# Kernel tuning notes

Hardware: AMD Instinct MI355X
Metric: run time of the kernel (lower is better)

## Reference

```python
import jax, jax.numpy as jnp
import numpy as np

N_NODES = 100000


def setup_inputs() -> dict:
    key = jax.random.key(0)
    k1, k2, k3, k4, k5 = jax.random.split(key, 5)
    in_f, out_f, E = 128, 128, 1600000
    std = 1.0 / np.sqrt(out_f)
    H = jax.random.normal(k1, (N_NODES, in_f), dtype=jnp.float32)
    W = jax.random.uniform(k2, (in_f, out_f), minval=-std, maxval=std, dtype=jnp.float32)
    bias = jax.random.uniform(k3, (out_f,), minval=-std, maxval=std, dtype=jnp.float32)
    row = jax.random.randint(k4, (E,), 0, N_NODES, dtype=jnp.int32)
    col = jax.random.randint(k5, (E,), 0, N_NODES, dtype=jnp.int32)
    return {"H": H, "W": W, "bias": bias, "row": row, "col": col}


def reference(H, W, bias, row, col):
    # H: [N, in_f]; W: [in_f, out_f]; row/col: [E] edge endpoints
    Hp = jnp.matmul(H, W)  # [N, out_f]
    # edge-wise attention: leaky_relu(<Hp[i], Hp[j]>)
    scores = jax.nn.leaky_relu(jnp.sum(Hp[row] * Hp[col], axis=-1), negative_slope=0.2)  # [E]
    # scatter-softmax over rows (matches sparse_softmax: exp / (row_sum + 1e-10))
    ex = jnp.exp(scores)
    denom = jax.ops.segment_sum(ex, row, num_segments=N_NODES)  # [N]
    attn = ex / (denom[row] + 1e-10)  # [E]
    # sparse-matmul aggregation: out[i] = sum_e attn[e] * Hp[col[e]]
    out = jax.ops.segment_sum(attn[:, None] * Hp[col], row, num_segments=N_NODES)  # [N, out_f]
    return out + bias
```

## Files before the change

kernel.cpp:

```cpp
#include <hip/hip_runtime.h>
#include <hip/hip_bf16.h>

#define RSH 7
#define RPB (1 << RSH)
#define CSH 17
#define CMASK ((1 << CSH) - 1)
#define CHUNK_E 8192
#define CAP 4096
#define NBMAX 1024

typedef __attribute__((ext_vector_type(8))) _Float16 f16x8;
typedef __attribute__((ext_vector_type(2))) _Float16 f16x2;
typedef __attribute__((ext_vector_type(4))) float f32x4;

__device__ __forceinline__ unsigned int pack2h(float a, float b) {
    union { _Float16 h[2]; unsigned int u; } c;
    c.h[0] = (_Float16)a; c.h[1] = (_Float16)b;
    return c.u;
}
__device__ __forceinline__ unsigned short f2h_bits(float f) {
    union { _Float16 h; unsigned short u; } c;
    c.h = (_Float16)f;
    return c.u;
}

__global__ __launch_bounds__(256) void wsplit(
    const float* __restrict__ Wg, unsigned int* __restrict__ WhiG)
{
    int task = blockIdx.x * 256 + threadIdx.x;
    if (task >= 2048) return;
    int n  = task & 127;
    int k0 = (task >> 7) * 8;
    unsigned int hi[4];
    #pragma unroll
    for (int j = 0; j < 4; ++j) {
        float w0 = Wg[(size_t)(k0 + 2*j)     * 128 + n];
        float w1 = Wg[(size_t)(k0 + 2*j + 1) * 128 + n];
        hi[j] = pack2h(w0, w1);
    }
    int byte = (k0 * 2) ^ ((n & 7) << 4);
    *(uint4*)((char*)WhiG + n * 256 + byte) = make_uint4(hi[0], hi[1], hi[2], hi[3]);
}

__global__ __launch_bounds__(512) void gemm_hist(
    const float* __restrict__ H, const unsigned int* __restrict__ WhiG,
    unsigned short* __restrict__ Hpb, int N,
    const int* __restrict__ row, unsigned short* __restrict__ Ht,
    int E, int nchunk, int nb2, int gemmBlocks)
{
    __shared__ unsigned short Ahi[128 * 128];
    __shared__ unsigned short Whi[128 * 128];
    const int tid = threadIdx.x;

    if (blockIdx.x >= gemmBlocks) {
        int* cnt = (int*)Ahi;
        const int c = blockIdx.x - gemmBlocks;
        for (int i = tid; i < nb2; i += 512) cnt[i] = 0;
        __syncthreads();
        const int e0 = c * CHUNK_E;
        const int e1 = min(e0 + CHUNK_E, E);
        for (int e = e0 + tid; e < e1; e += 512)
            atomicAdd(&cnt[row[e] >> RSH], 1);
        __syncthreads();
        for (int i = tid; i < nb2; i += 512)
            Ht[(size_t)i * nchunk + c] = (unsigned short)cnt[i];
        return;
    }

    const int rbase = blockIdx.x * 128;

    #pragma unroll
    for (int i = 0; i < 4; ++i) {
        int idx = tid + 512 * i;
        ((uint4*)Whi)[idx] = ((const uint4*)WhiG)[idx];
    }
    #pragma unroll
    for (int i = 0; i < 8; ++i) {
        int flat = tid + 512 * i;
        int rr = flat >> 5;
        int c4  = (flat & 31) * 4;
        float4 h = make_float4(0.f, 0.f, 0.f, 0.f);
        if (rbase + rr < N)
            h = *(const float4*)&H[(size_t)(rbase + rr) * 128 + c4];
        uint2 vh;
        vh.x = pack2h(h.x, h.y);
        vh.y = pack2h(h.z, h.w);
        int byte = (c4 * 2) ^ ((rr & 7) << 4);
        *(uint2*)((char*)Ahi + rr * 256 + byte) = vh;
    }
    __syncthreads();

    const int wid = tid >> 6, lane = tid & 63;
    const int wm = wid >> 1, wn = wid & 1;
    const int lr = lane & 15, lg = lane >> 4;
    f32x4 acc[2][4] = {};

    #pragma unroll
    for (int ks = 0; ks < 4; ++ks) {
        const int kb = ks * 64 + lg * 16;
        f16x8 ahi[2];
        #pragma unroll
        for (int mi = 0; mi < 2; ++mi) {
            int rr = wm * 32 + mi * 16 + lr;
            int sw = kb ^ ((rr & 7) << 4);
            ahi[mi] = *(const f16x8*)((char*)Ahi + rr * 256 + sw);
        }
        #pragma unroll
        for (int nf = 0; nf < 4; ++nf) {
            int n = wn * 64 + nf * 16 + lr;
            int sw = kb ^ ((n & 7) << 4);
            f16x8 bhi = *(const f16x8*)((char*)Whi + n * 256 + sw);
            #pragma unroll
            for (int mi = 0; mi < 2; ++mi)
                acc[mi][nf] = __builtin_amdgcn_mfma_f32_16x16x32_f16(ahi[mi], bhi, acc[mi][nf], 0, 0, 0);
        }
    }

    #pragma unroll
    for (int mi = 0; mi < 2; ++mi) {
        #pragma unroll
        for (int nf = 0; nf < 4; ++nf) {
            int col = wn * 64 + nf * 16 + lr;
            #pragma unroll
            for (int i = 0; i < 4; ++i) {
                int rr = rbase + wm * 32 + mi * 16 + lg * 4 + i;
                if (rr < N)
                    Hpb[(size_t)rr * 128 + col] = f2h_bits(acc[mi][nf][i]);
            }
        }
    }
}

__global__ __launch_bounds__(256) void bucket_scan(
    const unsigned short* __restrict__ Ht, unsigned short* __restrict__ rel,
    int* __restrict__ totals, int nchunk)
{
    __shared__ int s[256];
    const int b = blockIdx.x, tid = threadIdx.x;
    int v = (tid < nchunk) ? (int)Ht[(size_t)b * nchunk + tid] : 0;
    s[tid] = v;
    __syncthreads();
    for (int d = 1; d < 256; d <<= 1) {
        int t = (tid >= d) ? s[tid - d] : 0;
        __syncthreads();
        s[tid] += t;
        __syncthreads();
    }
    if (tid < nchunk) rel[(size_t)b * nchunk + tid] = (unsigned short)(s[tid] - v);
    if (tid == 255) totals[b] = s[255];
}

__global__ __launch_bounds__(1024) void bucket_ptr_scan(
    const int* __restrict__ totals, int* __restrict__ bucketptr, int nb2)
{
    __shared__ int s[1024];
    const int tid = threadIdx.x;
    int v = (tid < nb2) ? totals[tid] : 0;
    s[tid] = v;
    __syncthreads();
    for (int d = 1; d < 1024; d <<= 1) {
        int t = (tid >= d) ? s[tid - d] : 0;
        __syncthreads();
        s[tid] += t;
        __syncthreads();
    }
    if (tid < nb2) bucketptr[tid] = s[tid] - v;
    if (tid == nb2 - 1) bucketptr[nb2] = s[tid];
}

__global__ __launch_bounds__(256) void chunk_scatter(
    const int* __restrict__ row, const int* __restrict__ col,
    const unsigned short* __restrict__ rel, const int* __restrict__ bucketptr,
    int* __restrict__ colsort, int E, int nchunk, int nb2)
{
    __shared__ int cur[NBMAX];
    __shared__ int gb[NBMAX];
    const int tid = threadIdx.x;
    const int c = blockIdx.x;
    const int e0 = c * CHUNK_E;
    const int tot = min(CHUNK_E, E - e0);

    for (int b = tid; b < nb2; b += 256) {
        cur[b] = 0;
        gb[b] = bucketptr[b] + (int)rel[(size_t)b * nchunk + c];
    }
    __syncthreads();

    for (int j = tid; j < tot; j += 256) {
        int r = row[e0 + j], cc = col[e0 + j];
        int b = r >> RSH;
        int p = atomicAdd(&cur[b], 1);
        colsort[gb[b] + p] = ((r & (RPB - 1)) << CSH) | cc;
    }
}

__global__ __launch_bounds__(256) void bucket_sort(
    const int* __restrict__ bucketptr, int* __restrict__ rowptr,
    int* __restrict__ colsort, int N)
{
    __shared__ int rcnt[RPB];
    __shared__ int rcur[RPB];
    __shared__ int sc[256];
    __shared__ int ord[CAP];
    const int b = blockIdx.x, tid = threadIdx.x;
    const int rbase = b << RSH;
    const int s0 = bucketptr[b];
    const int cnt = bucketptr[b + 1] - s0;

    if (tid < RPB) rcnt[tid] = 0;
    __syncthreads();
    for (int j = tid; j < cnt; j += 256)
        atomicAdd(&rcnt[colsort[s0 + j] >> CSH], 1);
    __syncthreads();

    int v = (tid < RPB) ? rcnt[tid] : 0;
    sc[tid] = v;
    __syncthreads();
    for (int d = 1; d < RPB; d <<= 1) {
        int t = (tid >= d) ? sc[tid - d] : 0;
        __syncthreads();
        sc[tid] += t;
        __syncthreads();
    }
    if (tid < RPB) {
        int ex = sc[tid] - v;
        rcur[tid] = ex;
        int r = rbase + tid;
        if (r < N) rowptr[r] = s0 + ex;
    }
    if (tid == RPB - 1) {
        int rend = min(rbase + RPB, N);
        rowptr[rend] = s0 + cnt;
    }
    __syncthreads();

    for (int j = tid; j < cnt; j += 256) {
        int rec = colsort[s0 + j];
        int p = atomicAdd(&rcur[rec >> CSH], 1);
        ord[p] = rec & CMASK;
    }
    __syncthreads();
    for (int j = tid; j < cnt; j += 256)
        colsort[s0 + j] = ord[j];
}

union F16x8U {
    uint4 v;
    f16x2 p[4];
    _Float16 h[8];
};

__device__ __forceinline__ float dot8(const f16x2* a, const F16x8U& b) {
#if __has_builtin(__builtin_amdgcn_fdot2)
    float d = __builtin_amdgcn_fdot2(a[0], b.p[0], 0.f, false);
    d = __builtin_amdgcn_fdot2(a[1], b.p[1], d, false);
    d = __builtin_amdgcn_fdot2(a[2], b.p[2], d, false);
    d = __builtin_amdgcn_fdot2(a[3], b.p[3], d, false);
    return d;
#else
    float d = 0.f;
    #pragma unroll
    for (int k = 0; k < 8; ++k)
        d = fmaf((float)a[k >> 1][k & 1], (float)b.h[k], d);
    return d;
#endif
}

__global__ __launch_bounds__(256) void aggregate_kernel(
    const unsigned short* __restrict__ Hpb, const int* __restrict__ rowptr,
    const int* __restrict__ cols, const float* __restrict__ bias,
    float* __restrict__ out, int N)
{
    const int lane = threadIdx.x & 63;
    const int wv   = threadIdx.x >> 6;
    const int r = blockIdx.x * 4 + wv;
    if (r >= N) return;
    const int d = lane & 15;
    const int g = lane >> 4;

    const float4* bp = (const float4*)&bias[d * 8];
    const float4 b0 = bp[0], b1 = bp[1];

    F16x8U hru;
    hru.v = *(const uint4*)&Hpb[(size_t)r * 128 + d * 8];
    f16x2 hr2[4] = {hru.p[0], hru.p[1], hru.p[2], hru.p[3]};

    float acc[8] = {0.f,0.f,0.f,0.f,0.f,0.f,0.f,0.f};
    float den = 0.f;
    const int e0 = rowptr[r], e1 = rowptr[r + 1];
    const int elast = e1 - 1;

    for (int e = e0 + g; e < e1; e += 8) {
        const bool m1 = (e + 4 < e1);
        const int eb = m1 ? e + 4 : elast;
        int c0 = cols[e];
        int c1 = cols[eb];
        F16x8U u0, u1;
        u0.v = *(const uint4*)&Hpb[(size_t)c0 * 128 + d * 8];
        u1.v = *(const uint4*)&Hpb[(size_t)c1 * 128 + d * 8];

        float dot0 = dot8(hr2, u0);
        float dot1 = dot8(hr2, u1);

        dot0 += __shfl_xor(dot0, 1);
        dot1 += __shfl_xor(dot1, 1);
        dot0 += __shfl_xor(dot0, 2);
        dot1 += __shfl_xor(dot1, 2);
        dot0 += __shfl_xor(dot0, 4);
        dot1 += __shfl_xor(dot1, 4);
        dot0 += __shfl_xor(dot0, 8);
        dot1 += __shfl_xor(dot1, 8);

        float s0 = fmaxf(dot0, 0.2f * dot0);
        float s1 = fmaxf(dot1, 0.2f * dot1);
        float ex0 = __expf(s0);
        float ex1 = m1 ? __expf(s1) : 0.f;
        den += ex0 + ex1;
        #pragma unroll
        for (int k = 0; k < 8; ++k) {
            acc[k] = fmaf((float)u0.h[k], ex0, acc[k]);
            acc[k] = fmaf((float)u1.h[k], ex1, acc[k]);
        }
    }

    #pragma unroll
    for (int k = 0; k < 8; ++k) {
        acc[k] += __shfl_xor(acc[k], 16);
        acc[k] += __shfl_xor(acc[k], 32);
    }
    den += __shfl_xor(den, 16);
    den += __shfl_xor(den, 32);

    if (g == 0) {
        float inv = 1.f / (den + 1e-10f);
        float4 o0, o1;
        o0.x = fmaf(acc[0], inv, b0.x);
        o0.y = fmaf(acc[1], inv, b0.y);
        o0.z = fmaf(acc[2], inv, b0.z);
        o0.w = fmaf(acc[3], inv, b0.w);
        o1.x = fmaf(acc[4], inv, b1.x);
        o1.y = fmaf(acc[5], inv, b1.y);
        o1.z = fmaf(acc[6], inv, b1.z);
        o1.w = fmaf(acc[7], inv, b1.w);
        float4* op = (float4*)&out[(size_t)r * 128 + d * 8];
        op[0] = o0;
        op[1] = o1;
    }
}

extern "C" void kernel_launch(void* const* d_in, const int* in_sizes, int n_in,
                              void* d_out, int out_size, void* d_ws, size_t ws_size,
                              hipStream_t stream)
{
    const float* H    = (const float*)d_in[0];
    const float* W    = (const float*)d_in[1];
    const float* bias = (const float*)d_in[2];
    const int*   row  = (const int*)d_in[3];
    const int*   col  = (const int*)d_in[4];
    const int N = in_sizes[0] / 128;
    const int E = in_sizes[3];

    const int nchunk = (E + CHUNK_E - 1) / CHUNK_E;
    const int nb2    = (N + RPB - 1) / RPB;

    auto align = [](size_t x) { return (x + 255) & ~(size_t)255; };

    char* ws = (char*)d_ws;
    size_t off = 0;
    unsigned short* Hpb       = (unsigned short*)(ws + off); off = align(off + (size_t)N * 128 * 2);
    unsigned short* Ht        = (unsigned short*)(ws + off); off = align(off + (size_t)nb2 * nchunk * 2);
    unsigned short* rel       = (unsigned short*)(ws + off); off = align(off + (size_t)nb2 * nchunk * 2);
    int*            totals    = (int*)(ws + off);            off = align(off + (size_t)nb2 * 4);
    int*            bucketptr = (int*)(ws + off);            off = align(off + (size_t)(nb2 + 1) * 4);
    int*            rowptr    = (int*)(ws + off);            off = align(off + (size_t)(N + 1) * 4);
    unsigned int*   WhiG      = (unsigned int*)(ws + off);   off = align(off + 8192 * 4);
    int*            colsort   = (int*)(ws + off);

    const int gemmBlocks = (N + 127) / 128;

    wsplit<<<8, 256, 0, stream>>>(W, WhiG);
    gemm_hist<<<gemmBlocks + nchunk, 512, 0, stream>>>(H, WhiG, Hpb, N,
                                                       row, Ht, E, nchunk, nb2,
                                                       gemmBlocks);
    bucket_scan<<<nb2, 256, 0, stream>>>(Ht, rel, totals, nchunk);
    bucket_ptr_scan<<<1, 1024, 0, stream>>>(totals, bucketptr, nb2);
    chunk_scatter<<<nchunk, 256, 0, stream>>>(row, col, rel, bucketptr,
                                              colsort, E, nchunk, nb2);
    bucket_sort<<<nb2, 256, 0, stream>>>(bucketptr, rowptr, colsort, N);
    aggregate_kernel<<<(N + 3) / 4, 256, 0, stream>>>(Hpb, rowptr, colsort, bias,
                                                      (float*)d_out, N);
}
```

Baseline: 123.3 us.

## Fold weight conversion and bucket-pointer scan into neighbors; unroll aggregation 4x

The separate W conversion kernel is removed. Each GEMM block now converts W to swizzled fp16 in shared memory itself. The standalone bucket-pointer scan kernel is merged into bucket_scan via a last-block-done atomic counter, which gemm_hist resets. The aggregation loop now processes four edges per iteration instead of two, so more gathers are in flight. Together these cut two kernel launches and raise memory-level parallelism, at the cost of redundant W reads per GEMM block and higher register pressure in aggregation.

```diff
diff --git a/kernel.cpp b/kernel.cpp
--- a/kernel.cpp
+++ b/kernel.cpp
@@ -24,28 +24,11 @@
     return c.u;
 }
 
-__global__ __launch_bounds__(256) void wsplit(
-    const float* __restrict__ Wg, unsigned int* __restrict__ WhiG)
-{
-    int task = blockIdx.x * 256 + threadIdx.x;
-    if (task >= 2048) return;
-    int n  = task & 127;
-    int k0 = (task >> 7) * 8;
-    unsigned int hi[4];
-    #pragma unroll
-    for (int j = 0; j < 4; ++j) {
-        float w0 = Wg[(size_t)(k0 + 2*j)     * 128 + n];
-        float w1 = Wg[(size_t)(k0 + 2*j + 1) * 128 + n];
-        hi[j] = pack2h(w0, w1);
-    }
-    int byte = (k0 * 2) ^ ((n & 7) << 4);
-    *(uint4*)((char*)WhiG + n * 256 + byte) = make_uint4(hi[0], hi[1], hi[2], hi[3]);
-}
-
 __global__ __launch_bounds__(512) void gemm_hist(
-    const float* __restrict__ H, const unsigned int* __restrict__ WhiG,
+    const float* __restrict__ H, const float* __restrict__ Wg,
     unsigned short* __restrict__ Hpb, int N,
     const int* __restrict__ row, unsigned short* __restrict__ Ht,
+    int* __restrict__ scanctr,
     int E, int nchunk, int nb2, int gemmBlocks)
 {
     __shared__ unsigned short Ahi[128 * 128];
@@ -55,6 +38,7 @@
     if (blockIdx.x >= gemmBlocks) {
         int* cnt = (int*)Ahi;
         const int c = blockIdx.x - gemmBlocks;
+        if (c == 0 && tid == 0) *scanctr = 0;
         for (int i = tid; i < nb2; i += 512) cnt[i] = 0;
         __syncthreads();
         const int e0 = c * CHUNK_E;
@@ -71,8 +55,18 @@
 
     #pragma unroll
     for (int i = 0; i < 4; ++i) {
-        int idx = tid + 512 * i;
-        ((uint4*)Whi)[idx] = ((const uint4*)WhiG)[idx];
+        int task = tid + 512 * i;
+        int n  = task & 127;
+        int k0 = (task >> 7) * 8;
+        unsigned int hi[4];
+        #pragma unroll
+        for (int j = 0; j < 4; ++j) {
+            float w0 = Wg[(size_t)(k0 + 2*j)     * 128 + n];
+            float w1 = Wg[(size_t)(k0 + 2*j + 1) * 128 + n];
+            hi[j] = pack2h(w0, w1);
+        }
+        int byte = (k0 * 2) ^ ((n & 7) << 4);
+        *(uint4*)((char*)Whi + n * 256 + byte) = make_uint4(hi[0], hi[1], hi[2], hi[3]);
     }
     #pragma unroll
     for (int i = 0; i < 8; ++i) {
@@ -133,9 +127,11 @@
 
 __global__ __launch_bounds__(256) void bucket_scan(
     const unsigned short* __restrict__ Ht, unsigned short* __restrict__ rel,
-    int* __restrict__ totals, int nchunk)
+    int* __restrict__ totals, int* __restrict__ bucketptr,
+    int* __restrict__ scanctr, int nchunk, int nb2)
 {
     __shared__ int s[256];
+    __shared__ int lastFlag;
     const int b = blockIdx.x, tid = threadIdx.x;
     int v = (tid < nchunk) ? (int)Ht[(size_t)b * nchunk + tid] : 0;
     s[tid] = v;
@@ -147,25 +143,40 @@
         __syncthreads();
     }
     if (tid < nchunk) rel[(size_t)b * nchunk + tid] = (unsigned short)(s[tid] - v);
-    if (tid == 255) totals[b] = s[255];
-}
-
-__global__ __launch_bounds__(1024) void bucket_ptr_scan(
-    const int* __restrict__ totals, int* __restrict__ bucketptr, int nb2)
-{
-    __shared__ int s[1024];
-    const int tid = threadIdx.x;
-    int v = (tid < nb2) ? totals[tid] : 0;
-    s[tid] = v;
-    __syncthreads();
-    for (int d = 1; d < 1024; d <<= 1) {
+
+    if (tid == 0) {
+        totals[b] = s[255];
+        __threadfence();
+        lastFlag = (atomicAdd(scanctr, 1) == gridDim.x - 1);
+    }
+    __syncthreads();
+    if (!lastFlag) return;
+    __threadfence();
+
+    const int base4 = tid * 4;
+    int vv[4]; int sum = 0;
+    #pragma unroll
+    for (int i = 0; i < 4; ++i) {
+        int idx = base4 + i;
+        vv[i] = (idx < nb2) ? totals[idx] : 0;
+        sum += vv[i];
+    }
+    __syncthreads();
+    s[tid] = sum;
+    __syncthreads();
+    for (int d = 1; d < 256; d <<= 1) {
         int t = (tid >= d) ? s[tid - d] : 0;
         __syncthreads();
         s[tid] += t;
         __syncthreads();
     }
-    if (tid < nb2) bucketptr[tid] = s[tid] - v;
-    if (tid == nb2 - 1) bucketptr[nb2] = s[tid];
+    int run = s[tid] - sum;
+    #pragma unroll
+    for (int i = 0; i < 4; ++i) {
+        int idx = base4 + i;
+        if (idx < nb2) { bucketptr[idx] = run; run += vv[i]; }
+    }
+    if (tid == 255) bucketptr[nb2] = s[255];
 }
 
 __global__ __launch_bounds__(256) void chunk_scatter(
@@ -290,36 +301,57 @@
     const int e0 = rowptr[r], e1 = rowptr[r + 1];
     const int elast = e1 - 1;
 
-    for (int e = e0 + g; e < e1; e += 8) {
-        const bool m1 = (e + 4 < e1);
-        const int eb = m1 ? e + 4 : elast;
+    for (int e = e0 + g; e < e1; e += 16) {
+        const bool m1 = (e + 4  < e1);
+        const bool m2 = (e + 8  < e1);
+        const bool m3 = (e + 12 < e1);
         int c0 = cols[e];
-        int c1 = cols[eb];
-        F16x8U u0, u1;
+        int c1 = cols[m1 ? e + 4  : elast];
+        int c2 = cols[m2 ? e + 8  : elast];
+        int c3 = cols[m3 ? e + 12 : elast];
+        F16x8U u0, u1, u2, u3;
         u0.v = *(const uint4*)&Hpb[(size_t)c0 * 128 + d * 8];
         u1.v = *(const uint4*)&Hpb[(size_t)c1 * 128 + d * 8];
+        u2.v = *(const uint4*)&Hpb[(size_t)c2 * 128 + d * 8];
+        u3.v = *(const uint4*)&Hpb[(size_t)c3 * 128 + d * 8];
 
         float dot0 = dot8(hr2, u0);
         float dot1 = dot8(hr2, u1);
+        float dot2 = dot8(hr2, u2);
+        float dot3 = dot8(hr2, u3);
 
         dot0 += __shfl_xor(dot0, 1);
         dot1 += __shfl_xor(dot1, 1);
+        dot2 += __shfl_xor(dot2, 1);
+        dot3 += __shfl_xor(dot3, 1);
         dot0 += __shfl_xor(dot0, 2);
         dot1 += __shfl_xor(dot1, 2);
+        dot2 += __shfl_xor(dot2, 2);
+        dot3 += __shfl_xor(dot3, 2);
         dot0 += __shfl_xor(dot0, 4);
         dot1 += __shfl_xor(dot1, 4);
+        dot2 += __shfl_xor(dot2, 4);
+        dot3 += __shfl_xor(dot3, 4);
         dot0 += __shfl_xor(dot0, 8);
         dot1 += __shfl_xor(dot1, 8);
+        dot2 += __shfl_xor(dot2, 8);
+        dot3 += __shfl_xor(dot3, 8);
 
         float s0 = fmaxf(dot0, 0.2f * dot0);
         float s1 = fmaxf(dot1, 0.2f * dot1);
+        float s2 = fmaxf(dot2, 0.2f * dot2);
+        float s3 = fmaxf(dot3, 0.2f * dot3);
         float ex0 = __expf(s0);
         float ex1 = m1 ? __expf(s1) : 0.f;
-        den += ex0 + ex1;
+        float ex2 = m2 ? __expf(s2) : 0.f;
+        float ex3 = m3 ? __expf(s3) : 0.f;
+        den += (ex0 + ex1) + (ex2 + ex3);
         #pragma unroll
         for (int k = 0; k < 8; ++k) {
             acc[k] = fmaf((float)u0.h[k], ex0, acc[k]);
             acc[k] = fmaf((float)u1.h[k], ex1, acc[k]);
+            acc[k] = fmaf((float)u2.h[k], ex2, acc[k]);
+            acc[k] = fmaf((float)u3.h[k], ex3, acc[k]);
         }
     }
 
@@ -373,17 +405,16 @@
     int*            totals    = (int*)(ws + off);            off = align(off + (size_t)nb2 * 4);
     int*            bucketptr = (int*)(ws + off);            off = align(off + (size_t)(nb2 + 1) * 4);
     int*            rowptr    = (int*)(ws + off);            off = align(off + (size_t)(N + 1) * 4);
-    unsigned int*   WhiG      = (unsigned int*)(ws + off);   off = align(off + 8192 * 4);
+    int*            scanctr   = (int*)(ws + off);            off = align(off + 256);
     int*            colsort   = (int*)(ws + off);
 
     const int gemmBlocks = (N + 127) / 128;
 
-    wsplit<<<8, 256, 0, stream>>>(W, WhiG);
-    gemm_hist<<<gemmBlocks + nchunk, 512, 0, stream>>>(H, WhiG, Hpb, N,
-                                                       row, Ht, E, nchunk, nb2,
-                                                       gemmBlocks);
-    bucket_scan<<<nb2, 256, 0, stream>>>(Ht, rel, totals, nchunk);
-    bucket_ptr_scan<<<1, 1024, 0, stream>>>(totals, bucketptr, nb2);
+    gemm_hist<<<gemmBlocks + nchunk, 512, 0, stream>>>(H, W, Hpb, N,
+                                                       row, Ht, scanctr,
+                                                       E, nchunk, nb2, gemmBlocks);
+    bucket_scan<<<nb2, 256, 0, stream>>>(Ht, rel, totals, bucketptr,
+                                         scanctr, nchunk, nb2);
     chunk_scatter<<<nchunk, 256, 0, stream>>>(row, col, rel, bucketptr,
                                               colsort, E, nchunk, nb2);
     bucket_sort<<<nb2, 256, 0, stream>>>(bucketptr, rowptr, colsort, N);
```

Result: slower. 142.5 us (+15.6%).
